# Performance work log

Hardware: AMD Instinct MI355X
Metric: run time of the kernel (lower is better)

Reference implementation:

```python
import jax, jax.numpy as jnp
import numpy as np

K = 5          # kernel_size per pseudo-dim
DIM = 2        # pseudo-coordinate dim
N_NODES = 40000
N_EDGES = 640000
D = 64

# all 2^DIM linear B-spline corner offsets: [[0,0],[0,1],[1,0],[1,1]]
_BITS = jnp.array([[0, 0], [0, 1], [1, 0], [1, 1]], dtype=jnp.int32)  # [4,2]


def spline_basis(edge_attr):
    """Degree-1 open B-spline basis. Returns weights B [E,4] and kernel indices I [E,4]."""
    v = edge_attr * (K - 1.0)                       # [E,2], in [0, K-1]
    bot = jnp.clip(jnp.floor(v), 0.0, K - 2.0)      # clamp so bot+1 <= K-1
    frac = v - bot                                   # [E,2]
    w = jnp.where(_BITS[None].astype(bool), frac[:, None, :], 1.0 - frac[:, None, :])  # [E,4,2]
    B = w[..., 0] * w[..., 1]                        # [E,4]
    idx = bot.astype(jnp.int32)[:, None, :] + _BITS[None]  # [E,4,2]
    I = idx[..., 0] * K + idx[..., 1]                # [E,4] in [0,25)
    return B, I


def spline_conv(x, src, dst, B, I, W, root, bias, num_nodes):
    """SplineConv with max aggregation.
    x: [N,in], W: [25,in,out], root: [in,out], bias: [out]."""
    Y = jnp.einsum('ni,kio->nko', x, W)              # [N,25,out]
    gathered = Y[src[:, None], I]                    # [E,4,out]  (irregular gather)
    msg = jnp.einsum('es,eso->eo', B, gathered)      # [E,out]
    agg = jax.ops.segment_max(msg, dst, num_segments=num_nodes)  # [N,out]
    agg = jnp.where(jnp.isfinite(agg), agg, 0.0)     # empty segments -> 0 (PyG behavior)
    return agg + x @ root + bias


def setup_inputs() -> dict:
    key = jax.random.key(0)
    ks = jax.random.split(key, 9)
    x = jax.random.normal(ks[0], (N_NODES, D), dtype=jnp.float32)
    edge_index = jax.random.randint(ks[1], (2, N_EDGES), 0, N_NODES, dtype=jnp.int64)
    edge_attr = jax.random.uniform(ks[2], (N_EDGES, DIM), dtype=jnp.float32)
    s = 1.0 / np.sqrt(D * K * K)
    W1 = jax.random.normal(ks[3], (K * K, D, D), dtype=jnp.float32) * s
    root1 = jax.random.normal(ks[4], (D, D), dtype=jnp.float32) / np.sqrt(D)
    bias1 = jnp.zeros((D,), dtype=jnp.float32)
    W2 = jax.random.normal(ks[5], (K * K, D, D), dtype=jnp.float32) * s
    root2 = jax.random.normal(ks[6], (D, D), dtype=jnp.float32) / np.sqrt(D)
    bias2 = jnp.zeros((D,), dtype=jnp.float32)
    return {"x": x, "edge_index": edge_index, "edge_attr": edge_attr,
            "W1": W1, "root1": root1, "bias1": bias1,
            "W2": W2, "root2": root2, "bias2": bias2}


def reference(x, edge_index, edge_attr, W1, root1, bias1, W2, root2, bias2):
    src, dst = edge_index[0], edge_index[1]
    B, I = spline_basis(edge_attr)                   # shared by both layers
    h = spline_conv(x, src, dst, B, I, W1, root1, bias1, x.shape[0])
    h = jax.nn.relu(h)                               # ReLU after all but last layer
    out = spline_conv(h, src, dst, B, I, W2, root2, bias2, x.shape[0])
    return out
```

## Files before the change

kernel.cpp:

```cpp
#include <hip/hip_runtime.h>
#include <hip/hip_bf16.h>

#define E_N 640000
#define N_N 40000
#define SCAN_B 157

typedef __attribute__((ext_vector_type(8))) short short8;
typedef __attribute__((ext_vector_type(4))) float f32x4;

static __device__ __forceinline__ unsigned short f2bf(float f) {
  __hip_bfloat16 h = __float2bfloat16(f);
  unsigned short u;
  __builtin_memcpy(&u, &h, 2);
  return u;
}
static __device__ __forceinline__ float bf2f(unsigned short u) {
  return __uint_as_float(((unsigned int)u) << 16);
}

__global__ __launch_bounds__(256) void wtrans_kernel(
    const float* __restrict__ W1, const float* __restrict__ W2,
    unsigned short* __restrict__ Wt) {
  int t = blockIdx.x * 256 + threadIdx.x;
  int half = t >= 102400;
  int r = t - (half ? 102400 : 0);
  const float* W = half ? W2 : W1;
  int k = r >> 12, rr = r & 4095, o = rr >> 6, i = rr & 63;
  Wt[((size_t)half * 102400) + (k << 12) + (o << 6) + i] = f2bf(W[(k << 12) + (i << 6) + o]);
}

__global__ __launch_bounds__(256) void ygemm_kernel(
    const float* __restrict__ x, const unsigned short* __restrict__ Wt,
    unsigned short* __restrict__ Y) {
  __shared__ unsigned short tile[4][64 * 72];
  const int n0 = blockIdx.x * 64;
  const int w = threadIdx.x >> 6;
  const int l = threadIdx.x & 63;
  const int lr = l & 15;
  const int lh = l >> 4;
  unsigned short* tl = tile[w];

  short8 bx[4][2];
  #pragma unroll
  for (int nt = 0; nt < 4; ++nt) {
    const float* xp = x + ((size_t)(n0 + nt * 16 + lr) << 6) + (lh << 3);
    #pragma unroll
    for (int h = 0; h < 2; ++h) {
      float4 lo = *(const float4*)(xp + h * 32);
      float4 hi = *(const float4*)(xp + h * 32 + 4);
      short8 b;
      b[0] = (short)f2bf(lo.x); b[1] = (short)f2bf(lo.y);
      b[2] = (short)f2bf(lo.z); b[3] = (short)f2bf(lo.w);
      b[4] = (short)f2bf(hi.x); b[5] = (short)f2bf(hi.y);
      b[6] = (short)f2bf(hi.z); b[7] = (short)f2bf(hi.w);
      bx[nt][h] = b;
    }
  }

  const f32x4 Z = {0.0f, 0.0f, 0.0f, 0.0f};

  for (int k = w; k < 25; k += 4) {
    const unsigned short* wk = Wt + ((size_t)k << 12);
    short8 aw[4][2];
    #pragma unroll
    for (int ot = 0; ot < 4; ++ot)
      #pragma unroll
      for (int h = 0; h < 2; ++h)
        aw[ot][h] = *(const short8*)(wk + ((ot * 16 + lr) << 6) + (h << 5) + (lh << 3));

    f32x4 acc[4][4];
    #pragma unroll
    for (int ot = 0; ot < 4; ++ot)
      #pragma unroll
      for (int nt = 0; nt < 4; ++nt) {
        acc[ot][nt] = __builtin_amdgcn_mfma_f32_16x16x32_bf16(aw[ot][0], bx[nt][0], Z, 0, 0, 0);
        acc[ot][nt] = __builtin_amdgcn_mfma_f32_16x16x32_bf16(aw[ot][1], bx[nt][1], acc[ot][nt], 0, 0, 0);
      }

    #pragma unroll
    for (int ot = 0; ot < 4; ++ot)
      #pragma unroll
      for (int nt = 0; nt < 4; ++nt) {
        int node = nt * 16 + lr;
        int o = ot * 16 + (lh << 2);
        uint2 p;
        p.x = (unsigned)f2bf(acc[ot][nt][0]) | ((unsigned)f2bf(acc[ot][nt][1]) << 16);
        p.y = (unsigned)f2bf(acc[ot][nt][2]) | ((unsigned)f2bf(acc[ot][nt][3]) << 16);
        *(uint2*)(tl + node * 72 + o) = p;
      }

    #pragma unroll
    for (int r8 = 0; r8 < 8; ++r8) {
      int node = r8 * 8 + (l >> 3);
      int c = (l & 7) << 3;
      uint4 v = *(const uint4*)(tl + node * 72 + c);
      *(uint4*)(Y + ((size_t)(n0 + node) * 25 + k) * 64 + c) = v;
    }
  }
}

__global__ __launch_bounds__(256) void hist_kernel(
    const int* __restrict__ ei, int* __restrict__ cnt) {
  int e = blockIdx.x * 256 + threadIdx.x;
  atomicAdd(&cnt[ei[E_N + e]], 1);
}

__global__ __launch_bounds__(256) void scan1_kernel(
    const int* __restrict__ cnt, int* __restrict__ bsum) {
  __shared__ int red[256];
  int t = threadIdx.x;
  int j = blockIdx.x * 256 + t;
  red[t] = (j < N_N) ? cnt[j] : 0;
  __syncthreads();
  #pragma unroll
  for (int s = 128; s > 0; s >>= 1) {
    if (t < s) red[t] += red[t + s];
    __syncthreads();
  }
  if (t == 0) bsum[blockIdx.x] = red[0];
}

__global__ __launch_bounds__(256) void scan2_kernel(
    const int* __restrict__ bsum, int* __restrict__ bofs) {
  __shared__ int v[256];
  int t = threadIdx.x;
  v[t] = (t < SCAN_B) ? bsum[t] : 0;
  __syncthreads();
  if (t == 0) {
    int acc = 0;
    for (int i = 0; i < SCAN_B; ++i) { int c = v[i]; v[i] = acc; acc += c; }
  }
  __syncthreads();
  if (t < SCAN_B) bofs[t] = v[t];
}

__global__ __launch_bounds__(256) void scan3_kernel(
    int* __restrict__ cnt, const int* __restrict__ bofs,
    int* __restrict__ start) {
  __shared__ int v[2][256];
  int t = threadIdx.x;
  int j = blockIdx.x * 256 + t;
  int c = (j < N_N) ? cnt[j] : 0;
  v[0][t] = c;
  __syncthreads();
  int cur = 0;
  #pragma unroll
  for (int s = 1; s < 256; s <<= 1) {
    v[1 - cur][t] = (t >= s) ? v[cur][t] + v[cur][t - s] : v[cur][t];
    __syncthreads();
    cur = 1 - cur;
  }
  if (j < N_N) {
    int ex = bofs[blockIdx.x] + v[cur][t] - c;
    start[j] = ex;
    cnt[j] = ex;
    if (j == 0) start[N_N] = E_N;
  }
}

__global__ __launch_bounds__(256) void scatter_kernel(
    const float* __restrict__ ea, const int* __restrict__ ei,
    int* __restrict__ ofs, uint2* __restrict__ recs) {
  int e = blockIdx.x * 256 + threadIdx.x;
  int s = ei[e];
  int d = ei[E_N + e];
  float2 a = ((const float2*)ea)[e];
  float v0 = a.x * 4.0f, v1 = a.y * 4.0f;
  float b0f = fminf(fmaxf(floorf(v0), 0.0f), 3.0f);
  float b1f = fminf(fmaxf(floorf(v1), 0.0f), 3.0f);
  float f0 = v0 - b0f, f1 = v1 - b1f;
  int I0 = (int)b0f * 5 + (int)b1f;
  unsigned int q0 = (unsigned int)(f0 * 65535.0f + 0.5f);
  unsigned int q1 = (unsigned int)(f1 * 65535.0f + 0.5f);
  int pos = atomicAdd(&ofs[d], 1);
  uint2 rc;
  rc.x = (unsigned int)s | ((unsigned int)I0 << 16);
  rc.y = q0 | (q1 << 16);
  recs[pos] = rc;
}

static __device__ __forceinline__ float emsg(
    const unsigned short* __restrict__ Y, unsigned int rx, unsigned int ry, int lane) {
  int src = rx & 0xffff;
  int I0 = rx >> 16;
  float f0 = (float)(ry & 0xffff) * (1.0f / 65535.0f);
  float f1 = (float)(ry >> 16) * (1.0f / 65535.0f);
  const unsigned short* base = Y + (size_t)src * 1600 + I0 * 64 + lane;
  float y0 = bf2f(base[0]);
  float y1 = bf2f(base[64]);
  float y2 = bf2f(base[320]);
  float y3 = bf2f(base[384]);
  return (1.0f - f0) * ((1.0f - f1) * y0 + f1 * y1) +
         f0 * ((1.0f - f1) * y2 + f1 * y3);
}

__global__ __launch_bounds__(256) void agg_kernel(
    const unsigned short* __restrict__ Y, const uint2* __restrict__ recs,
    const int* __restrict__ start, const float* __restrict__ xin,
    const float* __restrict__ root, const float* __restrict__ bias,
    float* __restrict__ outp, int relu) {
  __shared__ float xl[4][64];
  const int w = threadIdx.x >> 6;
  const int lane = threadIdx.x & 63;
  const int n = blockIdx.x * 4 + w;
  xl[w][lane] = xin[((size_t)n << 6) + lane];
  __syncthreads();

  const int s = __builtin_amdgcn_readfirstlane(start[n]);
  const int e = __builtin_amdgcn_readfirstlane(start[n + 1]);
  const float NI = -__builtin_inff();
  float a0 = NI, a1 = NI, a2 = NI, a3 = NI;
  int j = s;
  for (; j + 4 <= e; j += 4) {
    uint2 r0 = recs[j];
    uint2 r1 = recs[j + 1];
    uint2 r2 = recs[j + 2];
    uint2 r3 = recs[j + 3];
    unsigned x0 = __builtin_amdgcn_readfirstlane(r0.x), y0 = __builtin_amdgcn_readfirstlane(r0.y);
    unsigned x1 = __builtin_amdgcn_readfirstlane(r1.x), y1 = __builtin_amdgcn_readfirstlane(r1.y);
    unsigned x2 = __builtin_amdgcn_readfirstlane(r2.x), y2 = __builtin_amdgcn_readfirstlane(r2.y);
    unsigned x3 = __builtin_amdgcn_readfirstlane(r3.x), y3 = __builtin_amdgcn_readfirstlane(r3.y);
    float m0 = emsg(Y, x0, y0, lane);
    float m1 = emsg(Y, x1, y1, lane);
    float m2 = emsg(Y, x2, y2, lane);
    float m3 = emsg(Y, x3, y3, lane);
    a0 = fmaxf(a0, m0);
    a1 = fmaxf(a1, m1);
    a2 = fmaxf(a2, m2);
    a3 = fmaxf(a3, m3);
  }
  for (; j < e; ++j) {
    uint2 rc = recs[j];
    unsigned rx = __builtin_amdgcn_readfirstlane(rc.x);
    unsigned ry = __builtin_amdgcn_readfirstlane(rc.y);
    a0 = fmaxf(a0, emsg(Y, rx, ry, lane));
  }
  float acc = fmaxf(fmaxf(a0, a1), fmaxf(a2, a3));
  if (s == e) acc = 0.0f;

  float r = bias[lane];
  #pragma unroll 8
  for (int i = 0; i < 64; ++i)
    r += xl[w][i] * root[(i << 6) + lane];
  r += acc;
  if (relu) r = fmaxf(r, 0.0f);
  outp[((size_t)n << 6) + lane] = r;
}

extern "C" void kernel_launch(void* const* d_in, const int* in_sizes, int n_in,
                              void* d_out, int out_size, void* d_ws, size_t ws_size,
                              hipStream_t stream) {
  const float* x = (const float*)d_in[0];
  const int* ei = (const int*)d_in[1];
  const float* ea = (const float*)d_in[2];
  const float* W1 = (const float*)d_in[3];
  const float* root1 = (const float*)d_in[4];
  const float* bias1 = (const float*)d_in[5];
  const float* W2 = (const float*)d_in[6];
  const float* root2 = (const float*)d_in[7];
  const float* bias2 = (const float*)d_in[8];
  float* out = (float*)d_out;

  const size_t yB = (size_t)N_N * 1600 * 2;
  const size_t rB = (size_t)E_N * 8;
  const size_t sB = (size_t)(N_N + 2) * 4;
  const size_t cB = (size_t)N_N * 4;
  const size_t wB = (size_t)2 * 25 * 64 * 64 * 2;
  const size_t bB = (size_t)1024 * 2;
  if (ws_size < yB + rB + sB + cB + wB + bB) return;

  char* p = (char*)d_ws;
  unsigned short* Y = (unsigned short*)p; p += yB;
  uint2* recs = (uint2*)p;                p += rB;
  int* startA = (int*)p;                  p += sB;
  int* cnt = (int*)p;                     p += cB;
  unsigned short* Wt = (unsigned short*)p; p += wB;
  int* bsum = (int*)p;                    p += 1024;
  int* bofs = (int*)p;
  float* h = out;

  unsigned short* Wt1 = Wt;
  unsigned short* Wt2 = Wt + (size_t)25 * 64 * 64;

  dim3 blk(256);

  hipMemsetAsync(cnt, 0, cB, stream);
  wtrans_kernel<<<800, blk, 0, stream>>>(W1, W2, Wt);
  hist_kernel<<<E_N / 256, blk, 0, stream>>>(ei, cnt);
  scan1_kernel<<<SCAN_B, blk, 0, stream>>>(cnt, bsum);
  scan2_kernel<<<1, blk, 0, stream>>>(bsum, bofs);
  scan3_kernel<<<SCAN_B, blk, 0, stream>>>(cnt, bofs, startA);
  scatter_kernel<<<E_N / 256, blk, 0, stream>>>(ea, ei, cnt, recs);

  ygemm_kernel<<<N_N / 64, blk, 0, stream>>>(x, Wt1, Y);
  agg_kernel<<<N_N / 4, blk, 0, stream>>>(Y, recs, startA, x, root1, bias1, h, 1);

  ygemm_kernel<<<N_N / 64, blk, 0, stream>>>(h, Wt2, Y);
  agg_kernel<<<N_N / 4, blk, 0, stream>>>(Y, recs, startA, h, root2, bias2, out, 0);
}
```

Baseline: 268.7 us.

## Make aggregation persistent with atomic work-stealing and prefetch next GEMM weights

The aggregation kernel becomes a persistent grid of 512 blocks. Each wave claims chunks of nodes through a global atomic counter, and the root matrix is staged once per block in shared memory instead of being read from global memory for every node. The counters are zeroed inside the weight-transpose kernel. The Y GEMM kernel also software-prefetches the next k-slice of weights while computing the current one. The goal is to cut block launch overhead, balance the uneven per-node degree, and hide weight-load latency, at the cost of atomic contention, more registers and lower occupancy from the 16KB of shared memory. There is also a possible shared-memory race on xl, since each wave writes its xl row without a barrier before reading it back.

New measurement: 672.5 us. 2.5x slower.

```diff
diff --git a/kernel.cpp b/kernel.cpp
--- a/kernel.cpp
+++ b/kernel.cpp
@@ -4,6 +4,8 @@
 #define E_N 640000
 #define N_N 40000
 #define SCAN_B 157
+#define AGG_BLOCKS 512
+#define CHUNK 2
 
 typedef __attribute__((ext_vector_type(8))) short short8;
 typedef __attribute__((ext_vector_type(4))) float f32x4;
@@ -20,7 +22,8 @@
 
 __global__ __launch_bounds__(256) void wtrans_kernel(
     const float* __restrict__ W1, const float* __restrict__ W2,
-    unsigned short* __restrict__ Wt) {
+    unsigned short* __restrict__ Wt, int* __restrict__ ctr) {
+  if (blockIdx.x == 0 && threadIdx.x < 2) ctr[threadIdx.x] = 0;
   int t = blockIdx.x * 256 + threadIdx.x;
   int half = t >= 102400;
   int r = t - (half ? 102400 : 0);
@@ -59,14 +62,28 @@
 
   const f32x4 Z = {0.0f, 0.0f, 0.0f, 0.0f};
 
-  for (int k = w; k < 25; k += 4) {
+  int k = w;
+  short8 aw[4][2];
+  {
     const unsigned short* wk = Wt + ((size_t)k << 12);
-    short8 aw[4][2];
     #pragma unroll
     for (int ot = 0; ot < 4; ++ot)
       #pragma unroll
       for (int h = 0; h < 2; ++h)
         aw[ot][h] = *(const short8*)(wk + ((ot * 16 + lr) << 6) + (h << 5) + (lh << 3));
+  }
+
+  while (k < 25) {
+    const int kn = k + 4;
+    short8 awn[4][2];
+    if (kn < 25) {
+      const unsigned short* wk = Wt + ((size_t)kn << 12);
+      #pragma unroll
+      for (int ot = 0; ot < 4; ++ot)
+        #pragma unroll
+        for (int h = 0; h < 2; ++h)
+          awn[ot][h] = *(const short8*)(wk + ((ot * 16 + lr) << 6) + (h << 5) + (lh << 3));
+    }
 
     f32x4 acc[4][4];
     #pragma unroll
@@ -96,6 +113,13 @@
       uint4 v = *(const uint4*)(tl + node * 72 + c);
       *(uint4*)(Y + ((size_t)(n0 + node) * 25 + k) * 64 + c) = v;
     }
+
+    #pragma unroll
+    for (int ot = 0; ot < 4; ++ot)
+      #pragma unroll
+      for (int h = 0; h < 2; ++h)
+        aw[ot][h] = awn[ot][h];
+    k = kn;
   }
 }
 
@@ -194,57 +218,70 @@
          f0 * ((1.0f - f1) * y2 + f1 * y3);
 }
 
-__global__ __launch_bounds__(256) void agg_kernel(
+__global__ __launch_bounds__(256, 8) void agg_kernel(
     const unsigned short* __restrict__ Y, const uint2* __restrict__ recs,
     const int* __restrict__ start, const float* __restrict__ xin,
     const float* __restrict__ root, const float* __restrict__ bias,
-    float* __restrict__ outp, int relu) {
+    float* __restrict__ outp, int relu, int* __restrict__ ctr) {
+  __shared__ float rl[64 * 64];
   __shared__ float xl[4][64];
   const int w = threadIdx.x >> 6;
   const int lane = threadIdx.x & 63;
-  const int n = blockIdx.x * 4 + w;
-  xl[w][lane] = xin[((size_t)n << 6) + lane];
-  __syncthreads();
-
-  const int s = __builtin_amdgcn_readfirstlane(start[n]);
-  const int e = __builtin_amdgcn_readfirstlane(start[n + 1]);
-  const float NI = -__builtin_inff();
-  float a0 = NI, a1 = NI, a2 = NI, a3 = NI;
-  int j = s;
-  for (; j + 4 <= e; j += 4) {
-    uint2 r0 = recs[j];
-    uint2 r1 = recs[j + 1];
-    uint2 r2 = recs[j + 2];
-    uint2 r3 = recs[j + 3];
-    unsigned x0 = __builtin_amdgcn_readfirstlane(r0.x), y0 = __builtin_amdgcn_readfirstlane(r0.y);
-    unsigned x1 = __builtin_amdgcn_readfirstlane(r1.x), y1 = __builtin_amdgcn_readfirstlane(r1.y);
-    unsigned x2 = __builtin_amdgcn_readfirstlane(r2.x), y2 = __builtin_amdgcn_readfirstlane(r2.y);
-    unsigned x3 = __builtin_amdgcn_readfirstlane(r3.x), y3 = __builtin_amdgcn_readfirstlane(r3.y);
-    float m0 = emsg(Y, x0, y0, lane);
-    float m1 = emsg(Y, x1, y1, lane);
-    float m2 = emsg(Y, x2, y2, lane);
-    float m3 = emsg(Y, x3, y3, lane);
-    a0 = fmaxf(a0, m0);
-    a1 = fmaxf(a1, m1);
-    a2 = fmaxf(a2, m2);
-    a3 = fmaxf(a3, m3);
-  }
-  for (; j < e; ++j) {
-    uint2 rc = recs[j];
-    unsigned rx = __builtin_amdgcn_readfirstlane(rc.x);
-    unsigned ry = __builtin_amdgcn_readfirstlane(rc.y);
-    a0 = fmaxf(a0, emsg(Y, rx, ry, lane));
-  }
-  float acc = fmaxf(fmaxf(a0, a1), fmaxf(a2, a3));
-  if (s == e) acc = 0.0f;
-
-  float r = bias[lane];
-  #pragma unroll 8
-  for (int i = 0; i < 64; ++i)
-    r += xl[w][i] * root[(i << 6) + lane];
-  r += acc;
-  if (relu) r = fmaxf(r, 0.0f);
-  outp[((size_t)n << 6) + lane] = r;
+  #pragma unroll
+  for (int r = 0; r < 16; ++r)
+    rl[threadIdx.x + 256 * r] = root[threadIdx.x + 256 * r];
+  const float bi = bias[lane];
+  __syncthreads();
+
+  for (;;) {
+    int base = 0;
+    if (lane == 0) base = atomicAdd(ctr, CHUNK);
+    base = __shfl(base, 0);
+    if (base >= N_N) break;
+    const int lim = (base + CHUNK < N_N) ? base + CHUNK : N_N;
+    for (int n = base; n < lim; ++n) {
+      xl[w][lane] = xin[((size_t)n << 6) + lane];
+      const int s = __builtin_amdgcn_readfirstlane(start[n]);
+      const int e = __builtin_amdgcn_readfirstlane(start[n + 1]);
+      const float NI = -__builtin_inff();
+      float a0 = NI, a1 = NI, a2 = NI, a3 = NI;
+      int j = s;
+      for (; j + 4 <= e; j += 4) {
+        uint2 r0 = recs[j];
+        uint2 r1 = recs[j + 1];
+        uint2 r2 = recs[j + 2];
+        uint2 r3 = recs[j + 3];
+        unsigned x0 = __builtin_amdgcn_readfirstlane(r0.x), y0 = __builtin_amdgcn_readfirstlane(r0.y);
+        unsigned x1 = __builtin_amdgcn_readfirstlane(r1.x), y1 = __builtin_amdgcn_readfirstlane(r1.y);
+        unsigned x2 = __builtin_amdgcn_readfirstlane(r2.x), y2 = __builtin_amdgcn_readfirstlane(r2.y);
+        unsigned x3 = __builtin_amdgcn_readfirstlane(r3.x), y3 = __builtin_amdgcn_readfirstlane(r3.y);
+        float m0 = emsg(Y, x0, y0, lane);
+        float m1 = emsg(Y, x1, y1, lane);
+        float m2 = emsg(Y, x2, y2, lane);
+        float m3 = emsg(Y, x3, y3, lane);
+        a0 = fmaxf(a0, m0);
+        a1 = fmaxf(a1, m1);
+        a2 = fmaxf(a2, m2);
+        a3 = fmaxf(a3, m3);
+      }
+      for (; j < e; ++j) {
+        uint2 rc = recs[j];
+        unsigned rx = __builtin_amdgcn_readfirstlane(rc.x);
+        unsigned ry = __builtin_amdgcn_readfirstlane(rc.y);
+        a0 = fmaxf(a0, emsg(Y, rx, ry, lane));
+      }
+      float acc = fmaxf(fmaxf(a0, a1), fmaxf(a2, a3));
+      if (s == e) acc = 0.0f;
+
+      float r = bi;
+      #pragma unroll 8
+      for (int i = 0; i < 64; ++i)
+        r += xl[w][i] * rl[(i << 6) + lane];
+      r += acc;
+      if (relu) r = fmaxf(r, 0.0f);
+      outp[((size_t)n << 6) + lane] = r;
+    }
+  }
 }
 
 extern "C" void kernel_launch(void* const* d_in, const int* in_sizes, int n_in,
@@ -266,7 +303,7 @@
   const size_t sB = (size_t)(N_N + 2) * 4;
   const size_t cB = (size_t)N_N * 4;
   const size_t wB = (size_t)2 * 25 * 64 * 64 * 2;
-  const size_t bB = (size_t)1024 * 2;
+  const size_t bB = (size_t)1024 * 2 + 64;
   if (ws_size < yB + rB + sB + cB + wB + bB) return;
 
   char* p = (char*)d_ws;
@@ -276,16 +313,17 @@
   int* cnt = (int*)p;                     p += cB;
   unsigned short* Wt = (unsigned short*)p; p += wB;
   int* bsum = (int*)p;                    p += 1024;
-  int* bofs = (int*)p;
+  int* bofs = (int*)p;                    p += 1024;
+  int* ctr = (int*)p;
+
   float* h = out;
-
   unsigned short* Wt1 = Wt;
   unsigned short* Wt2 = Wt + (size_t)25 * 64 * 64;
 
   dim3 blk(256);
 
   hipMemsetAsync(cnt, 0, cB, stream);
-  wtrans_kernel<<<800, blk, 0, stream>>>(W1, W2, Wt);
+  wtrans_kernel<<<800, blk, 0, stream>>>(W1, W2, Wt, ctr);
   hist_kernel<<<E_N / 256, blk, 0, stream>>>(ei, cnt);
   scan1_kernel<<<SCAN_B, blk, 0, stream>>>(cnt, bsum);
   scan2_kernel<<<1, blk, 0, stream>>>(bsum, bofs);
@@ -293,8 +331,8 @@
   scatter_kernel<<<E_N / 256, blk, 0, stream>>>(ea, ei, cnt, recs);
 
   ygemm_kernel<<<N_N / 64, blk, 0, stream>>>(x, Wt1, Y);
-  agg_kernel<<<N_N / 4, blk, 0, stream>>>(Y, recs, startA, x, root1, bias1, h, 1);
+  agg_kernel<<<AGG_BLOCKS, blk, 0, stream>>>(Y, recs, startA, x, root1, bias1, h, 1, ctr);
 
   ygemm_kernel<<<N_N / 64, blk, 0, stream>>>(h, Wt2, Y);
-  agg_kernel<<<N_N / 4, blk, 0, stream>>>(Y, recs, startA, h, root2, bias2, out, 0);
-}
+  agg_kernel<<<AGG_BLOCKS, blk, 0, stream>>>(Y, recs, startA, h, root2, bias2, out, 0, ctr + 1);
+}
```
